# Kernel optimization log

Hardware: AMD Instinct MI355X
Metric: run time of the kernel (lower is better)

## Reference

```python
import jax, jax.numpy as jnp
import numpy as np

N = 40000    # nodes
E = 400000   # edges
H = 128      # hidden_channels
G = 50       # num_gaussians
L = 3        # num_interactions
NG = 256     # number of graphs in the batch
CUTOFF = 6.0


def setup_inputs() -> dict:
    key = jax.random.key(0)
    ks = jax.random.split(key, 16)

    def w(k, shape, fan_in):
        return (jax.random.normal(k, shape, jnp.float32) / np.float32(np.sqrt(fan_in)))

    inp = {}
    inp["atomic_numbers"] = jax.random.randint(ks[0], (N,), 0, 100)
    inp["pos"] = jax.random.normal(ks[1], (N, 3), jnp.float32) * 5.0
    inp["edge_index"] = jax.random.randint(ks[2], (2, E), 0, N)
    inp["batch_ids"] = jnp.sort(jax.random.randint(ks[3], (N,), 0, NG))
    inp["embed"] = w(ks[4], (100, H), 1.0)
    inp["msg_w1"] = w(ks[5], (L, H, H), H)
    inp["msg_b1"] = jnp.zeros((L, H), jnp.float32)
    inp["msg_w2"] = w(ks[6], (L, H, 3 * H), H)
    inp["msg_b2"] = jnp.zeros((L, 3 * H), jnp.float32)
    inp["filt_w"] = w(ks[7], (L, G, 3 * H), G)
    inp["filt_b"] = jnp.zeros((L, 3 * H), jnp.float32)
    inp["vec_w"] = w(ks[8], (L, H, 2 * H), H)
    inp["upd_w1"] = w(ks[9], (L, 2 * H, H), 2 * H)
    inp["upd_b1"] = jnp.zeros((L, H), jnp.float32)
    inp["upd_w2"] = w(ks[10], (L, H, 3 * H), H)
    inp["upd_b2"] = jnp.zeros((L, 3 * H), jnp.float32)
    inp["ro_w1"] = w(ks[11], (H, H // 2), H)
    inp["ro_b1"] = jnp.zeros((H // 2,), jnp.float32)
    inp["ro_w2"] = w(ks[12], (H // 2, 1), H // 2)
    inp["ro_b2"] = jnp.zeros((1,), jnp.float32)
    return inp


def _painn(atomic_numbers, pos, edge_index, batch_ids, embed,
           msg_w1, msg_b1, msg_w2, msg_b2, filt_w, filt_b, vec_w,
           upd_w1, upd_b1, upd_w2, upd_b2, ro_w1, ro_b1, ro_w2, ro_b2):
    src, dst = edge_index[0], edge_index[1]
    n = atomic_numbers.shape[0]

    # geometry
    dvec = pos[src] - pos[dst]                              # [E,3]
    dist = jnp.linalg.norm(dvec, axis=-1)                   # [E]
    dvec_n = dvec / (dist[:, None] + 1e-8)                  # [E,3]

    # Gaussian smearing (RBF expansion of distances)
    offset = jnp.linspace(0.0, CUTOFF, G).astype(jnp.float32)
    coeff = -0.5 / (offset[1] - offset[0]) ** 2
    rbf = jnp.exp(coeff * (dist[:, None] - offset[None, :]) ** 2)  # [E,G]

    s = embed[atomic_numbers]                               # [N,H]
    v = jnp.zeros((n, 3, H), s.dtype)                       # [N,3,H]

    for i in range(L):
        # --- message block ---
        w = rbf @ filt_w[i] + filt_b[i]                     # [E,3H]
        s_all = jax.nn.relu(s @ msg_w1[i] + msg_b1[i]) @ msg_w2[i] + msg_b2[i]  # [N,3H]
        gate = s_all[src] * w                               # [E,3H]
        g0, g1, g2 = jnp.split(gate, 3, axis=-1)            # each [E,H]
        ds_e = g0
        dv_e = v[src] * g1[:, None, :] + dvec_n[:, :, None] * g2[:, None, :]  # [E,3,H]
        ds = jax.ops.segment_sum(ds_e, dst, num_segments=n)
        dv = jax.ops.segment_sum(dv_e, dst, num_segments=n)
        s = s + ds
        v = v + dv

        # --- update block ---
        vt = v @ vec_w[i]                                   # [N,3,2H]
        V1, V2 = jnp.split(vt, 2, axis=-1)                  # [N,3,H] each
        v_norm = jnp.linalg.norm(V1, axis=1)                # [N,H]
        u = (jax.nn.relu(jnp.concatenate([s, v_norm], axis=-1) @ upd_w1[i] + upd_b1[i])
             @ upd_w2[i] + upd_b2[i])                       # [N,3H]
        a, b, c = jnp.split(u, 3, axis=-1)
        s = s + a
        v = v * b[:, None, :] + V2 * c[:, None, :]

    # readout + global mean pool
    y = jax.nn.relu(s @ ro_w1 + ro_b1) @ ro_w2 + ro_b2      # [N,1]
    summed = jax.ops.segment_sum(y, batch_ids, num_segments=NG)
    counts = jax.ops.segment_sum(jnp.ones((n, 1), y.dtype), batch_ids, num_segments=NG)
    return summed / jnp.maximum(counts, 1.0)                # [NG,1]


def reference(atomic_numbers, pos, edge_index, batch_ids, embed,
              msg_w1, msg_b1, msg_w2, msg_b2, filt_w, filt_b, vec_w,
              upd_w1, upd_b1, upd_w2, upd_b2, ro_w1, ro_b1, ro_w2, ro_b2):
    return _painn(atomic_numbers, pos, edge_index, batch_ids, embed,
                  msg_w1, msg_b1, msg_w2, msg_b2, filt_w, filt_b, vec_w,
                  upd_w1, upd_b1, upd_w2, upd_b2, ro_w1, ro_b1, ro_w2, ro_b2)
```

## Files before the change

### kernel.cpp

```cpp
#include <hip/hip_runtime.h>
#include <hip/hip_bf16.h>
#include <math.h>


#define N_NODES 40000
#define N_EDGES 400000
#define NGAUSS  50
#define NLAY    3
#define NGRAPH  256

#define WS_BYTES (448ull * 1024 * 1024)
__device__ __align__(256) unsigned char g_ws[WS_BYTES];

typedef __attribute__((ext_vector_type(8))) short short8;
typedef __attribute__((ext_vector_type(4))) float f32x4;

__device__ __forceinline__ float relu_f(float x) { return fmaxf(x, 0.f); }
__device__ __forceinline__ unsigned short f2b(float x) {
  __hip_bfloat16 h = __float2bfloat16(x);
  return *reinterpret_cast<unsigned short*>(&h);
}
__device__ __forceinline__ float b2f(unsigned short u) {
  return __uint_as_float(((unsigned int)u) << 16);
}
__device__ __forceinline__ float b2f_lo(unsigned int u) {
  return __uint_as_float(u << 16);
}
__device__ __forceinline__ float b2f_hi(unsigned int u) {
  return __uint_as_float(u & 0xffff0000u);
}
__device__ __forceinline__ unsigned int pk(float a, float b) {
  return (unsigned int)f2b(a) | ((unsigned int)f2b(b) << 16);
}

__global__ __launch_bounds__(256) void cvt_kernel(const float* __restrict__ in,
                                                  unsigned short* __restrict__ out,
                                                  int n) {
  int i = blockIdx.x * 256 + threadIdx.x;
  if (i < n) out[i] = f2b(in[i]);
}

__global__ __launch_bounds__(256) void cvt_fw_kernel(const float* __restrict__ in,
                                                     unsigned short* __restrict__ out) {
  int idx = blockIdx.x * 256 + threadIdx.x;
  if (idx >= NLAY * NGAUSS * 384) return;
  int l = idx / (NGAUSS * 384);
  int rem = idx % (NGAUSS * 384);
  int g = rem / 384, c = rem % 384;
  int j = c >> 7, cc = c & 127;
  out[(size_t)l * NGAUSS * 384 + g * 384 + (cc >> 1) * 6 + j * 2 + (cc & 1)] =
      f2b(in[idx]);
}

__global__ __launch_bounds__(256) void geom_kernel(const int* __restrict__ src,
                                                   const int* __restrict__ dst,
                                                   const float* __restrict__ pos,
                                                   float4* __restrict__ geom) {
  int e = blockIdx.x * 256 + threadIdx.x;
  if (e >= N_EDGES) return;
  int s = src[e], d = dst[e];
  float dx = pos[s * 3 + 0] - pos[d * 3 + 0];
  float dy = pos[s * 3 + 1] - pos[d * 3 + 1];
  float dz = pos[s * 3 + 2] - pos[d * 3 + 2];
  float dist = sqrtf(dx * dx + dy * dy + dz * dz);
  float inv = 1.f / (dist + 1e-8f);
  geom[e] = make_float4(dx * inv, dy * inv, dz * inv, dist);
}

__global__ __launch_bounds__(256) void hist_kernel(const int* __restrict__ dst,
                                                   int* __restrict__ deg) {
  int e = blockIdx.x * 256 + threadIdx.x;
  if (e < N_EDGES) atomicAdd(&deg[dst[e]], 1);
}

__global__ __launch_bounds__(1024) void scan_kernel(const int* __restrict__ deg,
                                                    int* __restrict__ off, int n) {
  __shared__ int wsum[16];
  __shared__ int ctot;
  int t = threadIdx.x, lane = t & 63, w = t >> 6;
  int carry = 0;
  for (int base = 0; base < n; base += 1024) {
    int i = base + t;
    int v = (i < n) ? deg[i] : 0;
    int x = v;
#pragma unroll
    for (int dd = 1; dd < 64; dd <<= 1) {
      int y = __shfl_up(x, dd);
      if (lane >= dd) x += y;
    }
    if (lane == 63) wsum[w] = x;
    __syncthreads();
    if (w == 0 && lane < 16) {
      int self = wsum[lane];
      int xs = self;
#pragma unroll
      for (int dd = 1; dd < 16; dd <<= 1) {
        int y = __shfl_up(xs, dd);
        if (lane >= dd) xs += y;
      }
      wsum[lane] = xs - self;
      if (lane == 15) ctot = xs;
    }
    __syncthreads();
    if (i < n) off[i] = carry + wsum[w] + (x - v);
    carry += ctot;
    __syncthreads();
  }
  if (t == 0) off[n] = carry;
}

__global__ __launch_bounds__(256) void fill_kernel(const int* __restrict__ src,
                                                   const int* __restrict__ dst,
                                                   const int* __restrict__ off,
                                                   int* __restrict__ cursor,
                                                   const float4* __restrict__ geom,
                                                   int* __restrict__ srcs,
                                                   float4* __restrict__ geoms) {
  int e = blockIdx.x * 256 + threadIdx.x;
  if (e >= N_EDGES) return;
  int d = dst[e];
  int p = atomicAdd(&cursor[d], 1);
  int pos = off[d] + p;
  srcs[pos] = src[e];
  geoms[pos] = geom[e];
}

__global__ __launch_bounds__(256) void init_kernel(const int* __restrict__ z,
                                                   const float* __restrict__ embed,
                                                   float* __restrict__ s,
                                                   unsigned short* __restrict__ sb,
                                                   unsigned short* __restrict__ vax) {
  int idx = blockIdx.x * 256 + threadIdx.x;
  if (idx < N_NODES * 384) vax[idx] = 0;
  if (idx < N_NODES * 128) {
    int node = idx >> 7, c = idx & 127;
    float val = embed[z[node] * 128 + c];
    s[idx] = val;
    sb[idx] = f2b(val);
  }
}

#define KMAX 256
__global__ __launch_bounds__(256) void gemm_bf16(
    const unsigned short* __restrict__ A1, int lda1,
    const unsigned short* __restrict__ A2, int lda2, int kSplit,
    const unsigned short* __restrict__ B, int ldb,
    const float* __restrict__ bias,
    void* __restrict__ C, int ldc, int M, int K, int doRelu, int outMode) {
  __shared__ unsigned int Bt32[64][KMAX / 2 + 4];
  int t = threadIdx.x;
  int lane = t & 63, w = t >> 6;
  int n0 = blockIdx.x * 64, m0 = blockIdx.y * 128;
  {
    int c4 = (t & 15) * 4;
    for (int k = (t >> 4) * 2; k < K; k += 32) {
      uint2 va = *(const uint2*)&B[(size_t)k * ldb + n0 + c4];
      uint2 vb = *(const uint2*)&B[(size_t)(k + 1) * ldb + n0 + c4];
      Bt32[c4 + 0][k >> 1] = (va.x & 0xffffu) | (vb.x << 16);
      Bt32[c4 + 1][k >> 1] = (va.x >> 16) | (vb.x & 0xffff0000u);
      Bt32[c4 + 2][k >> 1] = (va.y & 0xffffu) | (vb.y << 16);
      Bt32[c4 + 3][k >> 1] = (va.y >> 16) | (vb.y & 0xffff0000u);
    }
  }
  __syncthreads();

  int row = lane & 15;
  int kg = lane >> 4;

  f32x4 acc[2][4];
#pragma unroll
  for (int rf = 0; rf < 2; ++rf)
#pragma unroll
    for (int nf = 0; nf < 4; ++nf) acc[rf][nf] = (f32x4){0.f, 0.f, 0.f, 0.f};

  for (int ks = 0; ks < K; ks += 32) {
    int kk = ks + kg * 8;
    short8 af[2];
#pragma unroll
    for (int rf = 0; rf < 2; ++rf) {
      int mrow = m0 + w * 32 + rf * 16 + row;
      if (mrow >= M) mrow = M - 1;
      const unsigned short* Ap;
      int kloc;
      if (kk < kSplit) { Ap = A1 + (size_t)mrow * lda1; kloc = kk; }
      else             { Ap = A2 + (size_t)mrow * lda2; kloc = kk - kSplit; }
      af[rf] = *(const short8*)&Ap[kloc];
    }
#pragma unroll
    for (int nf = 0; nf < 4; ++nf) {
      short8 bf = *(const short8*)((const unsigned short*)Bt32[nf * 16 + row] + kk);
#pragma unroll
      for (int rf = 0; rf < 2; ++rf)
        acc[rf][nf] = __builtin_amdgcn_mfma_f32_16x16x32_bf16(af[rf], bf,
                                                              acc[rf][nf], 0, 0, 0);
    }
  }

#pragma unroll
  for (int rf = 0; rf < 2; ++rf)
#pragma unroll
    for (int nf = 0; nf < 4; ++nf)
#pragma unroll
      for (int r = 0; r < 4; ++r) {
        int gr = m0 + w * 32 + rf * 16 + kg * 4 + r;
        int gc = n0 + nf * 16 + row;
        if (gr < M) {
          float val = acc[rf][nf][r] + (bias ? bias[gc] : 0.f);
          if (doRelu) val = relu_f(val);
          if (outMode == 0) {
            ((float*)C)[(size_t)gr * ldc + gc] = val;
          } else if (outMode == 1) {
            ((unsigned short*)C)[(size_t)gr * ldc + gc] = f2b(val);
          } else {
            int j = gc >> 7, cc = gc & 127;
            ((unsigned short*)C)[(size_t)gr * 384 + (cc >> 1) * 6 + j * 2 + (cc & 1)]
                = f2b(val);
          }
        }
      }
}

__global__ __launch_bounds__(256) void msg_kernel(const int* __restrict__ off,
                                                  const int* __restrict__ srcs,
                                                  const float4* __restrict__ geoms,
                                                  const unsigned int* __restrict__ s_allX,
                                                  const unsigned int* __restrict__ fwX,
                                                  const float* __restrict__ fb,
                                                  const float* __restrict__ s_in,
                                                  const unsigned int* __restrict__ vAx,
                                                  float* __restrict__ s_out,
                                                  unsigned short* __restrict__ s_out_b,
                                                  unsigned short* __restrict__ v_out_b) {
  int node = blockIdx.x * 4 + (threadIdx.x >> 6);
  if (node >= N_NODES) return;
  int lane = threadIdx.x & 63;
  int c2 = lane * 2;
  const float DELTA = 6.0f / 49.0f;
  const float INVD = 49.0f / 6.0f;
  const float CO = -0.5f * INVD * INVD;
  float fbr[3][2];
#pragma unroll
  for (int jj = 0; jj < 3; ++jj) {
    float2 f = *(const float2*)&fb[jj * 128 + c2];
    fbr[jj][0] = f.x; fbr[jj][1] = f.y;
  }
  float ds[2] = {0.f, 0.f};
  float dv[3][2] = {{0.f}};
  int e0 = off[node], e1 = off[node + 1];

  for (int q = e0; q < e1; ++q) {
    int s = srcs[q];
    float4 gm = geoms[q];
    float d = gm.w;
    float wv[3][2];
#pragma unroll
    for (int jj = 0; jj < 3; ++jj) { wv[jj][0] = fbr[jj][0]; wv[jj][1] = fbr[jj][1]; }
    int glo = max(0, (int)ceilf(d * INVD - 8.f));
    int ghi = min(NGAUSS - 1, (int)floorf(d * INVD + 8.f));
    for (int g = glo; g <= ghi; ++g) {
      float diff = d - g * DELTA;
      float r = __expf(CO * diff * diff);
      const unsigned int* fr = fwX + g * 192 + lane * 3;
      unsigned int f0 = fr[0], f1 = fr[1], f2v = fr[2];
      wv[0][0] = fmaf(r, b2f_lo(f0), wv[0][0]);
      wv[0][1] = fmaf(r, b2f_hi(f0), wv[0][1]);
      wv[1][0] = fmaf(r, b2f_lo(f1), wv[1][0]);
      wv[1][1] = fmaf(r, b2f_hi(f1), wv[1][1]);
      wv[2][0] = fmaf(r, b2f_lo(f2v), wv[2][0]);
      wv[2][1] = fmaf(r, b2f_hi(f2v), wv[2][1]);
    }
    const unsigned int* ps = s_allX + (size_t)s * 192 + lane * 3;
    const unsigned int* pv = vAx + (size_t)s * 192 + lane * 3;
    unsigned int s0 = ps[0], s1 = ps[1], s2 = ps[2];
    unsigned int v0 = pv[0], v1 = pv[1], v2 = pv[2];
    float gt[3][2];
    gt[0][0] = b2f_lo(s0) * wv[0][0];
    gt[0][1] = b2f_hi(s0) * wv[0][1];
    gt[1][0] = b2f_lo(s1) * wv[1][0];
    gt[1][1] = b2f_hi(s1) * wv[1][1];
    gt[2][0] = b2f_lo(s2) * wv[2][0];
    gt[2][1] = b2f_hi(s2) * wv[2][1];
    ds[0] += gt[0][0];
    ds[1] += gt[0][1];
    float dn[3] = {gm.x, gm.y, gm.z};
    unsigned int vvs[3] = {v0, v1, v2};
#pragma unroll
    for (int dd = 0; dd < 3; ++dd) {
      dv[dd][0] = fmaf(b2f_lo(vvs[dd]), gt[1][0], fmaf(dn[dd], gt[2][0], dv[dd][0]));
      dv[dd][1] = fmaf(b2f_hi(vvs[dd]), gt[1][1], fmaf(dn[dd], gt[2][1], dv[dd][1]));
    }
  }

  size_t sb = (size_t)node * 128 + c2;
  float2 si = *(const float2*)&s_in[sb];
  float2 so = make_float2(si.x + ds[0], si.y + ds[1]);
  *(float2*)&s_out[sb] = so;
  *(unsigned int*)&s_out_b[sb] = pk(so.x, so.y);
  const unsigned int* pv0 = vAx + (size_t)node * 192 + lane * 3;
  unsigned int vi0 = pv0[0], vi1 = pv0[1], vi2 = pv0[2];
  unsigned int vis[3] = {vi0, vi1, vi2};
#pragma unroll
  for (int dd = 0; dd < 3; ++dd) {
    size_t vb = (size_t)node * 384 + dd * 128 + c2;
    float vo0 = b2f_lo(vis[dd]) + dv[dd][0];
    float vo1 = b2f_hi(vis[dd]) + dv[dd][1];
    *(unsigned int*)&v_out_b[vb] = pk(vo0, vo1);
  }
}

__global__ __launch_bounds__(256) void vnorm_kernel(const unsigned short* __restrict__ V12b,
                                                    unsigned short* __restrict__ vnb) {
  int idx = blockIdx.x * 256 + threadIdx.x;
  if (idx >= N_NODES * 32) return;
  int node = idx >> 5, c4 = (idx & 31) * 4;
  size_t b = (size_t)node * 768 + c4;
  ushort4 x = *(const ushort4*)&V12b[b];
  ushort4 y = *(const ushort4*)&V12b[b + 256];
  ushort4 zz = *(const ushort4*)&V12b[b + 512];
  ushort4 o;
  o.x = f2b(sqrtf(b2f(x.x) * b2f(x.x) + b2f(y.x) * b2f(y.x) + b2f(zz.x) * b2f(zz.x)));
  o.y = f2b(sqrtf(b2f(x.y) * b2f(x.y) + b2f(y.y) * b2f(y.y) + b2f(zz.y) * b2f(zz.y)));
  o.z = f2b(sqrtf(b2f(x.z) * b2f(x.z) + b2f(y.z) * b2f(y.z) + b2f(zz.z) * b2f(zz.z)));
  o.w = f2b(sqrtf(b2f(x.w) * b2f(x.w) + b2f(y.w) * b2f(y.w) + b2f(zz.w) * b2f(zz.w)));
  *(ushort4*)&vnb[(size_t)node * 128 + c4] = o;
}

__global__ __launch_bounds__(256) void update_kernel(const float* __restrict__ s_msg,
                                                     const unsigned short* __restrict__ v_msg_b,
                                                     const unsigned short* __restrict__ u_b,
                                                     const unsigned short* __restrict__ V12b,
                                                     float* __restrict__ s_out,
                                                     unsigned short* __restrict__ s_out_b,
                                                     unsigned int* __restrict__ vAx) {
  int idx = blockIdx.x * 256 + threadIdx.x;
  if (idx >= N_NODES * 32) return;
  int node = idx >> 5, c4 = (idx & 31) * 4;
  size_t ub = (size_t)node * 384 + c4;
  ushort4 a4 = *(const ushort4*)&u_b[ub];
  ushort4 b4 = *(const ushort4*)&u_b[ub + 128];
  ushort4 c4v = *(const ushort4*)&u_b[ub + 256];
  size_t sb = (size_t)node * 128 + c4;
  float4 sm = *(const float4*)&s_msg[sb];
  float4 so = make_float4(sm.x + b2f(a4.x), sm.y + b2f(a4.y),
                          sm.z + b2f(a4.z), sm.w + b2f(a4.w));
  *(float4*)&s_out[sb] = so;
  ushort4 sob = {f2b(so.x), f2b(so.y), f2b(so.z), f2b(so.w)};
  *(ushort4*)&s_out_b[sb] = sob;
  float bb[4] = {b2f(b4.x), b2f(b4.y), b2f(b4.z), b2f(b4.w)};
  float cc[4] = {b2f(c4v.x), b2f(c4v.y), b2f(c4v.z), b2f(c4v.w)};
  int l0 = c4 >> 1;
#pragma unroll
  for (int dd = 0; dd < 3; ++dd) {
    size_t vb = (size_t)node * 384 + dd * 128 + c4;
    size_t vbv = (size_t)node * 768 + dd * 256 + 128 + c4;
    ushort4 vm = *(const ushort4*)&v_msg_b[vb];
    ushort4 v2 = *(const ushort4*)&V12b[vbv];
    float o0 = b2f(vm.x) * bb[0] + b2f(v2.x) * cc[0];
    float o1 = b2f(vm.y) * bb[1] + b2f(v2.y) * cc[1];
    float o2 = b2f(vm.z) * bb[2] + b2f(v2.z) * cc[2];
    float o3 = b2f(vm.w) * bb[3] + b2f(v2.w) * cc[3];
    vAx[(size_t)node * 192 + l0 * 3 + dd] = pk(o0, o1);
    vAx[(size_t)node * 192 + (l0 + 1) * 3 + dd] = pk(o2, o3);
  }
}

__global__ __launch_bounds__(256) void readout2_kernel(const float* __restrict__ ro_h,
                                                       const float* __restrict__ w2,
                                                       const int* __restrict__ batch,
                                                       float* __restrict__ pool,
                                                       float* __restrict__ cnt) {
  int node = blockIdx.x * 4 + (threadIdx.x >> 6);
  if (node >= N_NODES) return;
  int lane = threadIdx.x & 63;
  float y = ro_h[(size_t)node * 64 + lane] * w2[lane];
#pragma unroll
  for (int o = 32; o > 0; o >>= 1) y += __shfl_xor(y, o);
  if (lane == 0) {
    int b = batch[node];
    atomicAdd(&pool[b], y);
    atomicAdd(&cnt[b], 1.0f);
  }
}

__global__ void final_kernel(const float* __restrict__ pool,
                             const float* __restrict__ cnt,
                             const float* __restrict__ b2,
                             float* __restrict__ out) {
  int g = threadIdx.x;
  if (g < NGRAPH) out[g] = (pool[g] + cnt[g] * b2[0]) / fmaxf(cnt[g], 1.0f);
}

extern "C" void kernel_launch(void* const* d_in, const int* in_sizes, int n_in,
                              void* d_out, int out_size, void* d_ws, size_t ws_size,
                              hipStream_t stream) {
  const int*   z      = (const int*)d_in[0];
  const float* pos    = (const float*)d_in[1];
  const int*   esrc   = (const int*)d_in[2];
  const int*   edst   = esrc + N_EDGES;
  const int*   batch  = (const int*)d_in[3];
  const float* embed  = (const float*)d_in[4];
  const float* msg_w1 = (const float*)d_in[5];
  const float* msg_b1 = (const float*)d_in[6];
  const float* msg_w2 = (const float*)d_in[7];
  const float* msg_b2 = (const float*)d_in[8];
  const float* filt_w = (const float*)d_in[9];
  const float* filt_b = (const float*)d_in[10];
  const float* vec_w  = (const float*)d_in[11];
  const float* upd_w1 = (const float*)d_in[12];
  const float* upd_b1 = (const float*)d_in[13];
  const float* upd_w2 = (const float*)d_in[14];
  const float* upd_b2 = (const float*)d_in[15];
  const float* ro_w1  = (const float*)d_in[16];
  const float* ro_b1  = (const float*)d_in[17];
  const float* ro_w2  = (const float*)d_in[18];
  const float* ro_b2  = (const float*)d_in[19];
  (void)in_sizes; (void)n_in; (void)out_size;

  void* wsp = nullptr;
  if (hipGetSymbolAddress(&wsp, HIP_SYMBOL(g_ws)) != hipSuccess || wsp == nullptr) {
    wsp = d_ws;
  }
  char* wsb = (char*)wsp;
  size_t o = 0;
  auto alloc = [&](size_t bytes) -> void* {
    void* p = wsb + o;
    o += (bytes + 255) & ~(size_t)255;
    return p;
  };
  float4* geom   = (float4*)alloc(sizeof(float4) * N_EDGES);
  float4* geoms  = (float4*)alloc(sizeof(float4) * N_EDGES);
  int* srcs      = (int*)alloc(4ull * N_EDGES);
  int* csr_off   = (int*)alloc(4ull * (N_NODES + 1));
  int* deg       = (int*)alloc(4ull * N_NODES);
  int* cursor    = (int*)alloc(4ull * N_NODES);
  float* sA      = (float*)alloc(4ull * N_NODES * 128);
  float* sB      = (float*)alloc(4ull * N_NODES * 128);
  float* ro_h    = (float*)alloc(4ull * N_NODES * 64);
  unsigned short* s_allX = (unsigned short*)alloc(2ull * N_NODES * 384);
  unsigned short* sAb    = (unsigned short*)alloc(2ull * N_NODES * 128);
  unsigned short* sBb    = (unsigned short*)alloc(2ull * N_NODES * 128);
  unsigned short* vAx    = (unsigned short*)alloc(2ull * N_NODES * 384);
  unsigned short* vBb    = (unsigned short*)alloc(2ull * N_NODES * 384);
  unsigned short* vnb    = (unsigned short*)alloc(2ull * N_NODES * 128);
  unsigned short* hidden = (unsigned short*)alloc(2ull * N_NODES * 128);
  unsigned short* Vbuf_b = (unsigned short*)alloc(2ull * N_NODES * 768);
  unsigned short* ubuf_b = (unsigned short*)alloc(2ull * N_NODES * 384);
  unsigned short* wb_m1  = (unsigned short*)alloc(2ull * NLAY * 128 * 128);
  unsigned short* wb_m2  = (unsigned short*)alloc(2ull * NLAY * 128 * 384);
  unsigned short* wb_vw  = (unsigned short*)alloc(2ull * NLAY * 128 * 256);
  unsigned short* wb_u1  = (unsigned short*)alloc(2ull * NLAY * 256 * 128);
  unsigned short* wb_u2  = (unsigned short*)alloc(2ull * NLAY * 128 * 384);
  unsigned short* wb_fwX = (unsigned short*)alloc(2ull * NLAY * 50 * 384);
  unsigned short* wb_ro  = (unsigned short*)alloc(2ull * 128 * 64);
  float* pool    = (float*)alloc(4ull * NGRAPH);
  float* cnt     = (float*)alloc(4ull * NGRAPH);

  if (wsb == (char*)d_ws && o > ws_size) return;

  hipMemsetAsync(deg, 0, 4ull * N_NODES, stream);
  hipMemsetAsync(cursor, 0, 4ull * N_NODES, stream);
  hipMemsetAsync(pool, 0, 4ull * NGRAPH, stream);
  hipMemsetAsync(cnt, 0, 4ull * NGRAPH, stream);

  auto cvt = [&](const float* in, unsigned short* out, int n) {
    cvt_kernel<<<(n + 255) / 256, 256, 0, stream>>>(in, out, n);
  };
  cvt(msg_w1, wb_m1, NLAY * 128 * 128);
  cvt(msg_w2, wb_m2, NLAY * 128 * 384);
  cvt(vec_w,  wb_vw, NLAY * 128 * 256);
  cvt(upd_w1, wb_u1, NLAY * 256 * 128);
  cvt(upd_w2, wb_u2, NLAY * 128 * 384);
  cvt(ro_w1,  wb_ro, 128 * 64);
  cvt_fw_kernel<<<(NLAY * NGAUSS * 384 + 255) / 256, 256, 0, stream>>>(filt_w, wb_fwX);

  geom_kernel<<<(N_EDGES + 255) / 256, 256, 0, stream>>>(esrc, edst, pos, geom);
  hist_kernel<<<(N_EDGES + 255) / 256, 256, 0, stream>>>(edst, deg);
  scan_kernel<<<1, 1024, 0, stream>>>(deg, csr_off, N_NODES);
  fill_kernel<<<(N_EDGES + 255) / 256, 256, 0, stream>>>(esrc, edst, csr_off, cursor,
                                                         geom, srcs, geoms);
  init_kernel<<<(N_NODES * 384 + 255) / 256, 256, 0, stream>>>(z, embed, sA, sAb, vAx);

  const int BIG = 1 << 30;
  const int GY40 = (N_NODES + 127) / 128;
  const int GY120 = (N_NODES * 3 + 127) / 128;
  for (int i = 0; i < NLAY; ++i) {
    const float* mb1 = msg_b1 + (size_t)i * 128;
    const float* mb2 = msg_b2 + (size_t)i * 384;
    const float* fbv = filt_b + (size_t)i * 384;
    const float* ub1 = upd_b1 + (size_t)i * 128;
    const float* ub2 = upd_b2 + (size_t)i * 384;
    const unsigned short* m1 = wb_m1 + (size_t)i * 128 * 128;
    const unsigned short* m2 = wb_m2 + (size_t)i * 128 * 384;
    const unsigned short* vw = wb_vw + (size_t)i * 128 * 256;
    const unsigned short* u1 = wb_u1 + (size_t)i * 256 * 128;
    const unsigned short* u2 = wb_u2 + (size_t)i * 128 * 384;
    const unsigned int* fwX = (const unsigned int*)(wb_fwX + (size_t)i * 50 * 384);

    gemm_bf16<<<dim3(2, GY40), 256, 0, stream>>>(sAb, 128, sAb, 128, BIG, m1, 128, mb1,
                                                 hidden, 128, N_NODES, 128, 1, 1);
    gemm_bf16<<<dim3(6, GY40), 256, 0, stream>>>(hidden, 128, hidden, 128, BIG, m2, 384,
                                                 mb2, s_allX, 384, N_NODES, 128, 0, 2);
    msg_kernel<<<N_NODES / 4, 256, 0, stream>>>(csr_off, srcs, geoms,
                                                (const unsigned int*)s_allX, fwX, fbv,
                                                sA, (const unsigned int*)vAx,
                                                sB, sBb, vBb);
    gemm_bf16<<<dim3(4, GY120), 256, 0, stream>>>(vBb, 128, vBb, 128, BIG, vw, 256,
                                                  nullptr, Vbuf_b, 256, N_NODES * 3,
                                                  128, 0, 1);
    vnorm_kernel<<<(N_NODES * 32 + 255) / 256, 256, 0, stream>>>(Vbuf_b, vnb);
    gemm_bf16<<<dim3(2, GY40), 256, 0, stream>>>(sBb, 128, vnb, 128, 128, u1, 128, ub1,
                                                 hidden, 128, N_NODES, 256, 1, 1);
    gemm_bf16<<<dim3(6, GY40), 256, 0, stream>>>(hidden, 128, hidden, 128, BIG, u2, 384,
                                                 ub2, ubuf_b, 384, N_NODES, 128, 0, 1);
    update_kernel<<<(N_NODES * 32 + 255) / 256, 256, 0, stream>>>(sB, vBb, ubuf_b,
                                                                  Vbuf_b, sA, sAb,
                                                                  (unsigned int*)vAx);
  }

  gemm_bf16<<<dim3(1, GY40), 256, 0, stream>>>(sAb, 128, sAb, 128, BIG, wb_ro, 64,
                                               ro_b1, ro_h, 64, N_NODES, 128, 1, 0);
  readout2_kernel<<<N_NODES / 4, 256, 0, stream>>>(ro_h, ro_w2, batch, pool, cnt);
  final_kernel<<<1, 256, 0, stream>>>(pool, cnt, ro_b2, (float*)d_out);
}
```

Baseline: 1.264 ms.

## Merge weight conversions into one kernel, parallelize CSR scan, pre-permute msg_w2

Seven weight-conversion launches are replaced by one kernel that also writes msg_w2 and msg_b2 in the interleaved column order msg_kernel expects. The GEMM epilogue therefore drops its scattered permuted-store mode and uses plain row-major bf16 stores. The single-block 1024-thread scan over 40k nodes becomes a three-kernel block-parallel scan. The goal is less launch overhead, less serial scan time and simpler GEMM stores, at the cost of two extra scan launches.

```diff
diff --git a/kernel.cpp b/kernel.cpp
--- a/kernel.cpp
+++ b/kernel.cpp
@@ -32,24 +32,60 @@
 __device__ __forceinline__ unsigned int pk(float a, float b) {
   return (unsigned int)f2b(a) | ((unsigned int)f2b(b) << 16);
 }
-
-__global__ __launch_bounds__(256) void cvt_kernel(const float* __restrict__ in,
-                                                  unsigned short* __restrict__ out,
-                                                  int n) {
+__device__ __forceinline__ int perm384(int c) {
+  int j = c >> 7, cc = c & 127;
+  return (cc >> 1) * 6 + j * 2 + (cc & 1);
+}
+
+#define S0 (NLAY * 128 * 128)
+#define S1 (NLAY * 128 * 384)
+#define S2 (NLAY * 128 * 256)
+#define S3 (NLAY * 256 * 128)
+#define S4 (NLAY * 128 * 384)
+#define S5 (NLAY * NGAUSS * 384)
+#define S6 (128 * 64)
+#define S7 (NLAY * 384)
+#define S_TOT (S0 + S1 + S2 + S3 + S4 + S5 + S6 + S7)
+
+__global__ __launch_bounds__(256) void cvt_all_kernel(
+    const float* __restrict__ m1i, const float* __restrict__ m2i,
+    const float* __restrict__ vwi, const float* __restrict__ u1i,
+    const float* __restrict__ u2i, const float* __restrict__ fwi,
+    const float* __restrict__ roi, const float* __restrict__ mb2i,
+    unsigned short* __restrict__ m1o, unsigned short* __restrict__ m2o,
+    unsigned short* __restrict__ vwo, unsigned short* __restrict__ u1o,
+    unsigned short* __restrict__ u2o, unsigned short* __restrict__ fwo,
+    unsigned short* __restrict__ roo, float* __restrict__ mb2o) {
   int i = blockIdx.x * 256 + threadIdx.x;
-  if (i < n) out[i] = f2b(in[i]);
-}
-
-__global__ __launch_bounds__(256) void cvt_fw_kernel(const float* __restrict__ in,
-                                                     unsigned short* __restrict__ out) {
-  int idx = blockIdx.x * 256 + threadIdx.x;
-  if (idx >= NLAY * NGAUSS * 384) return;
-  int l = idx / (NGAUSS * 384);
-  int rem = idx % (NGAUSS * 384);
-  int g = rem / 384, c = rem % 384;
-  int j = c >> 7, cc = c & 127;
-  out[(size_t)l * NGAUSS * 384 + g * 384 + (cc >> 1) * 6 + j * 2 + (cc & 1)] =
-      f2b(in[idx]);
+  if (i >= S_TOT) return;
+  if (i < S0) { m1o[i] = f2b(m1i[i]); return; }
+  i -= S0;
+  if (i < S1) {
+    int l = i / (128 * 384), rem = i % (128 * 384);
+    int r = rem / 384, c = rem % 384;
+    m2o[(size_t)l * 128 * 384 + r * 384 + perm384(c)] = f2b(m2i[i]);
+    return;
+  }
+  i -= S1;
+  if (i < S2) { vwo[i] = f2b(vwi[i]); return; }
+  i -= S2;
+  if (i < S3) { u1o[i] = f2b(u1i[i]); return; }
+  i -= S3;
+  if (i < S4) { u2o[i] = f2b(u2i[i]); return; }
+  i -= S4;
+  if (i < S5) {
+    int l = i / (NGAUSS * 384), rem = i % (NGAUSS * 384);
+    int g = rem / 384, c = rem % 384;
+    fwo[(size_t)l * NGAUSS * 384 + g * 384 + perm384(c)] = f2b(fwi[i]);
+    return;
+  }
+  i -= S5;
+  if (i < S6) { roo[i] = f2b(roi[i]); return; }
+  i -= S6;
+  {
+    int l = i / 384, c = i % 384;
+    mb2o[l * 384 + perm384(c)] = mb2i[i];
+  }
 }
 
 __global__ __launch_bounds__(256) void geom_kernel(const int* __restrict__ src,
@@ -73,40 +109,57 @@
   if (e < N_EDGES) atomicAdd(&deg[dst[e]], 1);
 }
 
-__global__ __launch_bounds__(1024) void scan_kernel(const int* __restrict__ deg,
-                                                    int* __restrict__ off, int n) {
-  __shared__ int wsum[16];
-  __shared__ int ctot;
-  int t = threadIdx.x, lane = t & 63, w = t >> 6;
+#define SCAN_NB ((N_NODES + 255) / 256)
+__global__ __launch_bounds__(256) void scan_a(const int* __restrict__ deg,
+                                              int* __restrict__ bsum) {
+  __shared__ int red[4];
+  int b = blockIdx.x, t = threadIdx.x;
+  int i = b * 256 + t;
+  int x = (i < N_NODES) ? deg[i] : 0;
+#pragma unroll
+  for (int o = 32; o > 0; o >>= 1) x += __shfl_xor(x, o);
+  if ((t & 63) == 0) red[t >> 6] = x;
+  __syncthreads();
+  if (t == 0) bsum[b] = red[0] + red[1] + red[2] + red[3];
+}
+
+__global__ __launch_bounds__(64) void scan_b(const int* __restrict__ bsum,
+                                             int* __restrict__ boff) {
+  int lane = threadIdx.x;
   int carry = 0;
-  for (int base = 0; base < n; base += 1024) {
-    int i = base + t;
-    int v = (i < n) ? deg[i] : 0;
+  for (int base = 0; base < SCAN_NB; base += 64) {
+    int i = base + lane;
+    int v = (i < SCAN_NB) ? bsum[i] : 0;
     int x = v;
 #pragma unroll
-    for (int dd = 1; dd < 64; dd <<= 1) {
-      int y = __shfl_up(x, dd);
-      if (lane >= dd) x += y;
+    for (int d = 1; d < 64; d <<= 1) {
+      int y = __shfl_up(x, d);
+      if (lane >= d) x += y;
     }
-    if (lane == 63) wsum[w] = x;
-    __syncthreads();
-    if (w == 0 && lane < 16) {
-      int self = wsum[lane];
-      int xs = self;
-#pragma unroll
-      for (int dd = 1; dd < 16; dd <<= 1) {
-        int y = __shfl_up(xs, dd);
-        if (lane >= dd) xs += y;
-      }
-      wsum[lane] = xs - self;
-      if (lane == 15) ctot = xs;
-    }
-    __syncthreads();
-    if (i < n) off[i] = carry + wsum[w] + (x - v);
-    carry += ctot;
-    __syncthreads();
-  }
-  if (t == 0) off[n] = carry;
+    if (i < SCAN_NB) boff[i] = carry + x - v;
+    carry += __shfl(x, 63);
+  }
+}
+
+__global__ __launch_bounds__(256) void scan_c(const int* __restrict__ deg,
+                                              const int* __restrict__ boff,
+                                              int* __restrict__ off) {
+  __shared__ int woff[4];
+  int b = blockIdx.x, t = threadIdx.x, lane = t & 63, w = t >> 6;
+  int i = b * 256 + t;
+  int v = (i < N_NODES) ? deg[i] : 0;
+  int x = v;
+#pragma unroll
+  for (int d = 1; d < 64; d <<= 1) {
+    int y = __shfl_up(x, d);
+    if (lane >= d) x += y;
+  }
+  if (lane == 63) woff[w] = x;
+  __syncthreads();
+  int add = 0;
+  for (int k = 0; k < w; ++k) add += woff[k];
+  if (i < N_NODES) off[i] = boff[b] + add + x - v;
+  if (b == 0 && t == 0) off[N_NODES] = N_EDGES;
 }
 
 __global__ __launch_bounds__(256) void fill_kernel(const int* __restrict__ src,
@@ -207,15 +260,8 @@
         if (gr < M) {
           float val = acc[rf][nf][r] + (bias ? bias[gc] : 0.f);
           if (doRelu) val = relu_f(val);
-          if (outMode == 0) {
-            ((float*)C)[(size_t)gr * ldc + gc] = val;
-          } else if (outMode == 1) {
-            ((unsigned short*)C)[(size_t)gr * ldc + gc] = f2b(val);
-          } else {
-            int j = gc >> 7, cc = gc & 127;
-            ((unsigned short*)C)[(size_t)gr * 384 + (cc >> 1) * 6 + j * 2 + (cc & 1)]
-                = f2b(val);
-          }
+          if (outMode == 0) ((float*)C)[(size_t)gr * ldc + gc] = val;
+          else              ((unsigned short*)C)[(size_t)gr * ldc + gc] = f2b(val);
         }
       }
 }
@@ -433,9 +479,12 @@
   int* csr_off   = (int*)alloc(4ull * (N_NODES + 1));
   int* deg       = (int*)alloc(4ull * N_NODES);
   int* cursor    = (int*)alloc(4ull * N_NODES);
+  int* bsum      = (int*)alloc(4ull * SCAN_NB);
+  int* boff      = (int*)alloc(4ull * SCAN_NB);
   float* sA      = (float*)alloc(4ull * N_NODES * 128);
   float* sB      = (float*)alloc(4ull * N_NODES * 128);
   float* ro_h    = (float*)alloc(4ull * N_NODES * 64);
+  float* mb2p    = (float*)alloc(4ull * NLAY * 384);
   unsigned short* s_allX = (unsigned short*)alloc(2ull * N_NODES * 384);
   unsigned short* sAb    = (unsigned short*)alloc(2ull * N_NODES * 128);
   unsigned short* sBb    = (unsigned short*)alloc(2ull * N_NODES * 128);
@@ -445,13 +494,13 @@
   unsigned short* hidden = (unsigned short*)alloc(2ull * N_NODES * 128);
   unsigned short* Vbuf_b = (unsigned short*)alloc(2ull * N_NODES * 768);
   unsigned short* ubuf_b = (unsigned short*)alloc(2ull * N_NODES * 384);
-  unsigned short* wb_m1  = (unsigned short*)alloc(2ull * NLAY * 128 * 128);
-  unsigned short* wb_m2  = (unsigned short*)alloc(2ull * NLAY * 128 * 384);
-  unsigned short* wb_vw  = (unsigned short*)alloc(2ull * NLAY * 128 * 256);
-  unsigned short* wb_u1  = (unsigned short*)alloc(2ull * NLAY * 256 * 128);
-  unsigned short* wb_u2  = (unsigned short*)alloc(2ull * NLAY * 128 * 384);
-  unsigned short* wb_fwX = (unsigned short*)alloc(2ull * NLAY * 50 * 384);
-  unsigned short* wb_ro  = (unsigned short*)alloc(2ull * 128 * 64);
+  unsigned short* wb_m1  = (unsigned short*)alloc(2ull * S0);
+  unsigned short* wb_m2  = (unsigned short*)alloc(2ull * S1);
+  unsigned short* wb_vw  = (unsigned short*)alloc(2ull * S2);
+  unsigned short* wb_u1  = (unsigned short*)alloc(2ull * S3);
+  unsigned short* wb_u2  = (unsigned short*)alloc(2ull * S4);
+  unsigned short* wb_fwX = (unsigned short*)alloc(2ull * S5);
+  unsigned short* wb_ro  = (unsigned short*)alloc(2ull * S6);
   float* pool    = (float*)alloc(4ull * NGRAPH);
   float* cnt     = (float*)alloc(4ull * NGRAPH);
 
@@ -462,20 +511,15 @@
   hipMemsetAsync(pool, 0, 4ull * NGRAPH, stream);
   hipMemsetAsync(cnt, 0, 4ull * NGRAPH, stream);
 
-  auto cvt = [&](const float* in, unsigned short* out, int n) {
-    cvt_kernel<<<(n + 255) / 256, 256, 0, stream>>>(in, out, n);
-  };
-  cvt(msg_w1, wb_m1, NLAY * 128 * 128);
-  cvt(msg_w2, wb_m2, NLAY * 128 * 384);
-  cvt(vec_w,  wb_vw, NLAY * 128 * 256);
-  cvt(upd_w1, wb_u1, NLAY * 256 * 128);
-  cvt(upd_w2, wb_u2, NLAY * 128 * 384);
-  cvt(ro_w1,  wb_ro, 128 * 64);
-  cvt_fw_kernel<<<(NLAY * NGAUSS * 384 + 255) / 256, 256, 0, stream>>>(filt_w, wb_fwX);
+  cvt_all_kernel<<<(S_TOT + 255) / 256, 256, 0, stream>>>(
+      msg_w1, msg_w2, vec_w, upd_w1, upd_w2, filt_w, ro_w1, msg_b2,
+      wb_m1, wb_m2, wb_vw, wb_u1, wb_u2, wb_fwX, wb_ro, mb2p);
 
   geom_kernel<<<(N_EDGES + 255) / 256, 256, 0, stream>>>(esrc, edst, pos, geom);
   hist_kernel<<<(N_EDGES + 255) / 256, 256, 0, stream>>>(edst, deg);
-  scan_kernel<<<1, 1024, 0, stream>>>(deg, csr_off, N_NODES);
+  scan_a<<<SCAN_NB, 256, 0, stream>>>(deg, bsum);
+  scan_b<<<1, 64, 0, stream>>>(bsum, boff);
+  scan_c<<<SCAN_NB, 256, 0, stream>>>(deg, boff, csr_off);
   fill_kernel<<<(N_EDGES + 255) / 256, 256, 0, stream>>>(esrc, edst, csr_off, cursor,
                                                          geom, srcs, geoms);
   init_kernel<<<(N_NODES * 384 + 255) / 256, 256, 0, stream>>>(z, embed, sA, sAb, vAx);
@@ -485,7 +529,7 @@
   const int GY120 = (N_NODES * 3 + 127) / 128;
   for (int i = 0; i < NLAY; ++i) {
     const float* mb1 = msg_b1 + (size_t)i * 128;
-    const float* mb2 = msg_b2 + (size_t)i * 384;
+    const float* mb2i = mb2p + (size_t)i * 384;
     const float* fbv = filt_b + (size_t)i * 384;
     const float* ub1 = upd_b1 + (size_t)i * 128;
     const float* ub2 = upd_b2 + (size_t)i * 384;
@@ -499,7 +543,7 @@
     gemm_bf16<<<dim3(2, GY40), 256, 0, stream>>>(sAb, 128, sAb, 128, BIG, m1, 128, mb1,
                                                  hidden, 128, N_NODES, 128, 1, 1);
     gemm_bf16<<<dim3(6, GY40), 256, 0, stream>>>(hidden, 128, hidden, 128, BIG, m2, 384,
-                                                 mb2, s_allX, 384, N_NODES, 128, 0, 2);
+                                                 mb2i, s_allX, 384, N_NODES, 128, 0, 1);
     msg_kernel<<<N_NODES / 4, 256, 0, stream>>>(csr_off, srcs, geoms,
                                                 (const unsigned int*)s_allX, fwX, fbv,
                                                 sA, (const unsigned int*)vAx,
```

After: 1.182 ms. 6.5% less time.
